# Kernel optimization log

Measured on AMD Instinct MI355X. Metric: run time of the kernel, lower is better.

## Reference

```python
import jax, jax.numpy as jnp
import numpy as np

_FRAC_BITS = 8  # assumed fixed-point fractional bits for bits_quant
_SCALE = float(2 ** _FRAC_BITS)

def bits_quant(x):
    # Simulated fixed-point quantization: round to nearest multiple of 2^-8.
    return jnp.round(x * _SCALE) / _SCALE


def setup_inputs() -> dict:
    key = jax.random.key(0)
    k1, k2, k3 = jax.random.split(key, 3)
    B, D_in, D_out = 4096, 4096, 4096
    inputs = jax.random.normal(k1, (B, D_in), dtype=jnp.float32)
    w = jax.random.normal(k2, (D_in, D_out), dtype=jnp.float32) * 0.02
    b = jax.random.normal(k3, (D_out,), dtype=jnp.float32) * 0.02
    return {"inputs": inputs, "w": w, "b": b}


def reference(inputs, w, b):
    # y = bits_quant(inputs @ w) + bits_quant(b); out = bits_quant(y)
    y = bits_quant(jnp.matmul(inputs, w)) + bits_quant(b)
    return bits_quant(y)
```

## Files before the change

kernel.cpp:

```cpp
#include <hip/hip_runtime.h>
#include <math.h>

typedef __attribute__((ext_vector_type(8)))  short  short8;
typedef __attribute__((ext_vector_type(16))) float  f32x16;
typedef __attribute__((ext_vector_type(4)))  float  float4v;
typedef __attribute__((ext_vector_type(8)))  unsigned short ushort8;
typedef __attribute__((ext_vector_type(4)))  unsigned short ushort4v;

#define NDIM 4096
#define BM 256
#define BN 128
#define BK 64

__device__ __forceinline__ unsigned short f2bf(float f) {
  unsigned u = __builtin_bit_cast(unsigned, f);
  u += 0x7fffu + ((u >> 16) & 1u);
  return (unsigned short)(u >> 16);
}

__device__ __forceinline__ void gload_lds16(const unsigned short* g, unsigned short* l) {
  __builtin_amdgcn_global_load_lds(
      (const __attribute__((address_space(1))) void*)g,
      (__attribute__((address_space(3))) void*)l, 16, 0, 0);
}

__global__ void prep(const float* __restrict__ A, unsigned short* __restrict__ Abf,
                     const float* __restrict__ W, unsigned short* __restrict__ Wt) {
  __shared__ unsigned short tileb[64][68];
  const int t = threadIdx.x;
  if (blockIdx.x < 8192) {
    int i = (blockIdx.x * 256 + t) * 8;
    float4v a = *(const float4v*)(A + i);
    float4v b = *(const float4v*)(A + i + 4);
    ushort8 o;
    o[0] = f2bf(a[0]); o[1] = f2bf(a[1]); o[2] = f2bf(a[2]); o[3] = f2bf(a[3]);
    o[4] = f2bf(b[0]); o[5] = f2bf(b[1]); o[6] = f2bf(b[2]); o[7] = f2bf(b[3]);
    *(ushort8*)(Abf + i) = o;
  } else {
    int b  = blockIdx.x - 8192;
    int n0 = (b & 63) * 64, k0 = (b >> 6) * 64;
    const int rr = t >> 4;
    const int cc = (t & 15) * 4;
#pragma unroll
    for (int i = 0; i < 4; ++i) {
      int k = rr + i * 16;
      float4v v = *(const float4v*)&W[(size_t)(k0 + k) * NDIM + n0 + cc];
      ushort4v u;
      u[0] = f2bf(v[0]); u[1] = f2bf(v[1]); u[2] = f2bf(v[2]); u[3] = f2bf(v[3]);
      *(ushort4v*)&tileb[k][cc] = u;
    }
    __syncthreads();
#pragma unroll
    for (int i = 0; i < 2; ++i) {
      int c  = t + i * 256;
      int n  = c >> 3;
      int kc = (c & 7) * 8;
      ushort8 v;
#pragma unroll
      for (int j = 0; j < 8; ++j) v[j] = tileb[kc + j][n];
      *(ushort8*)&Wt[(size_t)(n0 + n) * NDIM + k0 + kc] = v;
    }
  }
}

__global__ __launch_bounds__(256, 2)
void gemm_bt_quant(const unsigned short* __restrict__ A,
                   const unsigned short* __restrict__ Bt,
                   const float* __restrict__ bias,
                   float* __restrict__ C) {
  __shared__ unsigned short As[BM * BK];
  __shared__ unsigned short Bs[BN * BK];

  const int tid  = threadIdx.x;
  const int lane = tid & 63;
  const int wid  = tid >> 6;
  const int wm   = (wid >> 1) * 128;
  const int wn   = (wid & 1) * 64;
  const int m0   = blockIdx.y * BM;
  const int n0   = blockIdx.x * BN;

  const int srow = tid >> 3;
  const int sc   = (tid & 7) ^ (srow & 7);
  const unsigned short* Ag = A  + (size_t)(m0 + srow) * NDIM + sc * 8;
  const unsigned short* Bg = Bt + (size_t)(n0 + srow) * NDIM + sc * 8;

  const int fr = lane & 31;
  const int fh = lane >> 5;
  const int fsw = fr & 7;

  f32x16 acc[4][2] = {};

  for (int kt = 0; kt < NDIM; kt += BK) {
#pragma unroll
    for (int p = 0; p < 8; ++p)
      gload_lds16(Ag + kt + (size_t)(p * 32) * NDIM, &As[(p * 256 + tid) * 8]);
#pragma unroll
    for (int p = 0; p < 4; ++p)
      gload_lds16(Bg + kt + (size_t)(p * 32) * NDIM, &Bs[(p * 256 + tid) * 8]);
    __syncthreads();

#pragma unroll
    for (int h = 0; h < 4; ++h) {
      const int cph = (2 * h + fh) ^ fsw;
      short8 af[4], bfr[2];
#pragma unroll
      for (int i = 0; i < 4; ++i)
        af[i] = *(const short8*)&As[(wm + i * 32 + fr) * BK + cph * 8];
#pragma unroll
      for (int j = 0; j < 2; ++j)
        bfr[j] = *(const short8*)&Bs[(wn + j * 32 + fr) * BK + cph * 8];
#pragma unroll
      for (int i = 0; i < 4; ++i)
#pragma unroll
        for (int j = 0; j < 2; ++j)
          acc[i][j] = __builtin_amdgcn_mfma_f32_32x32x16_bf16(af[i], bfr[j], acc[i][j], 0, 0, 0);
    }
    __syncthreads();
  }

  const float inv = 1.0f / 256.0f;
#pragma unroll
  for (int j = 0; j < 2; ++j) {
    const int col = n0 + wn + j * 32 + fr;
    const float qb = rintf(bias[col] * 256.0f) * inv;
#pragma unroll
    for (int i = 0; i < 4; ++i) {
      const int rb = m0 + wm + i * 32 + 4 * fh;
#pragma unroll
      for (int r = 0; r < 16; ++r) {
        const int row = rb + (r & 3) + 8 * (r >> 2);
        C[(size_t)row * NDIM + col] = rintf(acc[i][j][r] * 256.0f) * inv + qb;
      }
    }
  }
}

__global__ void gemm_fb(const float* __restrict__ A, const float* __restrict__ W,
                        const float* __restrict__ bias, float* __restrict__ C) {
  __shared__ float As[32][33], Ws[32][33];
  int tx = threadIdx.x, ty = threadIdx.y;
  int m0 = blockIdx.y * 32, n0 = blockIdx.x * 32;
  float acc[4] = {0.f, 0.f, 0.f, 0.f};
  for (int k0 = 0; k0 < NDIM; k0 += 32) {
#pragma unroll
    for (int i = 0; i < 4; ++i) {
      int r = ty + i * 8;
      As[r][tx] = A[(size_t)(m0 + r) * NDIM + k0 + tx];
      Ws[r][tx] = W[(size_t)(k0 + r) * NDIM + n0 + tx];
    }
    __syncthreads();
#pragma unroll
    for (int k = 0; k < 32; ++k) {
      float wv = Ws[k][tx];
#pragma unroll
      for (int i = 0; i < 4; ++i) acc[i] += As[ty + i * 8][k] * wv;
    }
    __syncthreads();
  }
  float qb = rintf(bias[n0 + tx] * 256.0f) * (1.0f / 256.0f);
#pragma unroll
  for (int i = 0; i < 4; ++i)
    C[(size_t)(m0 + ty + i * 8) * NDIM + n0 + tx] =
        rintf(acc[i] * 256.0f) * (1.0f / 256.0f) + qb;
}

extern "C" void kernel_launch(void* const* d_in, const int* in_sizes, int n_in,
                              void* d_out, int out_size, void* d_ws, size_t ws_size,
                              hipStream_t stream) {
  const float* A    = (const float*)d_in[0];
  const float* W    = (const float*)d_in[1];
  const float* bias = (const float*)d_in[2];
  float* C = (float*)d_out;
  const size_t nElem = (size_t)NDIM * NDIM;

  if (ws_size >= nElem * 4) {
    unsigned short* Abf = (unsigned short*)d_ws;
    unsigned short* Wt  = Abf + nElem;
    prep<<<8192 + 4096, 256, 0, stream>>>(A, Abf, W, Wt);
    gemm_bt_quant<<<dim3(NDIM / BN, NDIM / BM), 256, 0, stream>>>(Abf, Wt, bias, C);
  } else {
    gemm_fb<<<dim3(128, 128), dim3(32, 8), 0, stream>>>(A, W, bias, C);
  }
}
```

Measured before the change: 299.5 us.

## Double-buffer LDS tiles and enlarge GEMM block tile to 256x256

```diff
diff --git a/kernel.cpp b/kernel.cpp
--- a/kernel.cpp
+++ b/kernel.cpp
@@ -9,7 +9,7 @@
 
 #define NDIM 4096
 #define BM 256
-#define BN 128
+#define BN 256
 #define BK 64
 
 __device__ __forceinline__ unsigned short f2bf(float f) {
@@ -63,19 +63,19 @@
   }
 }
 
-__global__ __launch_bounds__(256, 2)
+__global__ __launch_bounds__(256, 1)
 void gemm_bt_quant(const unsigned short* __restrict__ A,
                    const unsigned short* __restrict__ Bt,
                    const float* __restrict__ bias,
                    float* __restrict__ C) {
-  __shared__ unsigned short As[BM * BK];
-  __shared__ unsigned short Bs[BN * BK];
+  __shared__ unsigned short As[2][BM * BK];
+  __shared__ unsigned short Bs[2][BN * BK];
 
   const int tid  = threadIdx.x;
   const int lane = tid & 63;
   const int wid  = tid >> 6;
   const int wm   = (wid >> 1) * 128;
-  const int wn   = (wid & 1) * 64;
+  const int wn   = (wid & 1) * 128;
   const int m0   = blockIdx.y * BM;
   const int n0   = blockIdx.x * BN;
 
@@ -84,43 +84,57 @@
   const unsigned short* Ag = A  + (size_t)(m0 + srow) * NDIM + sc * 8;
   const unsigned short* Bg = Bt + (size_t)(n0 + srow) * NDIM + sc * 8;
 
-  const int fr = lane & 31;
-  const int fh = lane >> 5;
+  const int fr  = lane & 31;
+  const int fh  = lane >> 5;
   const int fsw = fr & 7;
 
-  f32x16 acc[4][2] = {};
+  f32x16 acc[4][4] = {};
 
-  for (int kt = 0; kt < NDIM; kt += BK) {
-#pragma unroll
-    for (int p = 0; p < 8; ++p)
-      gload_lds16(Ag + kt + (size_t)(p * 32) * NDIM, &As[(p * 256 + tid) * 8]);
-#pragma unroll
-    for (int p = 0; p < 4; ++p)
-      gload_lds16(Bg + kt + (size_t)(p * 32) * NDIM, &Bs[(p * 256 + tid) * 8]);
+#define STAGE(buf, koff)                                                        \
+  _Pragma("unroll")                                                             \
+  for (int p = 0; p < 8; ++p) {                                                 \
+    gload_lds16(Ag + (koff) + (size_t)(p * 32) * NDIM,                          \
+                &As[buf][(p * 256 + tid) * 8]);                                 \
+    gload_lds16(Bg + (koff) + (size_t)(p * 32) * NDIM,                          \
+                &Bs[buf][(p * 256 + tid) * 8]);                                 \
+  }
+
+#define COMPUTE(buf)                                                            \
+  _Pragma("unroll")                                                             \
+  for (int h = 0; h < 4; ++h) {                                                 \
+    const int cph = (2 * h + fh) ^ fsw;                                         \
+    short8 af[4], bfr[4];                                                       \
+    _Pragma("unroll")                                                           \
+    for (int i = 0; i < 4; ++i)                                                 \
+      af[i] = *(const short8*)&As[buf][(wm + i * 32 + fr) * BK + cph * 8];      \
+    _Pragma("unroll")                                                           \
+    for (int j = 0; j < 4; ++j)                                                 \
+      bfr[j] = *(const short8*)&Bs[buf][(wn + j * 32 + fr) * BK + cph * 8];     \
+    _Pragma("unroll")                                                           \
+    for (int i = 0; i < 4; ++i)                                                 \
+      _Pragma("unroll")                                                         \
+      for (int j = 0; j < 4; ++j)                                               \
+        acc[i][j] = __builtin_amdgcn_mfma_f32_32x32x16_bf16(af[i], bfr[j],      \
+                                                            acc[i][j], 0, 0, 0);\
+  }
+
+  STAGE(0, 0);
+  for (int kt = 0; kt < NDIM; kt += 2 * BK) {
     __syncthreads();
-
-#pragma unroll
-    for (int h = 0; h < 4; ++h) {
-      const int cph = (2 * h + fh) ^ fsw;
-      short8 af[4], bfr[2];
-#pragma unroll
-      for (int i = 0; i < 4; ++i)
-        af[i] = *(const short8*)&As[(wm + i * 32 + fr) * BK + cph * 8];
-#pragma unroll
-      for (int j = 0; j < 2; ++j)
-        bfr[j] = *(const short8*)&Bs[(wn + j * 32 + fr) * BK + cph * 8];
-#pragma unroll
-      for (int i = 0; i < 4; ++i)
-#pragma unroll
-        for (int j = 0; j < 2; ++j)
-          acc[i][j] = __builtin_amdgcn_mfma_f32_32x32x16_bf16(af[i], bfr[j], acc[i][j], 0, 0, 0);
-    }
+    STAGE(1, kt + BK);
+    COMPUTE(0);
     __syncthreads();
+    int kn = kt + 2 * BK;
+    if (kn >= NDIM) kn = 0;
+    STAGE(0, kn);
+    COMPUTE(1);
   }
+#undef STAGE
+#undef COMPUTE
 
   const float inv = 1.0f / 256.0f;
 #pragma unroll
-  for (int j = 0; j < 2; ++j) {
+  for (int j = 0; j < 4; ++j) {
     const int col = n0 + wn + j * 32 + fr;
     const float qb = rintf(bias[col] * 256.0f) * inv;
 #pragma unroll
```

After: 317.6 us. +6.0%, slower.
